# Kernel tuning notes

Measured on AMD Instinct MI355X. Metric: run time of the kernel, lower is better.

Reference implementation:

```python
import jax, jax.numpy as jnp
import numpy as np

C_IN, CH, HCH, NFFT, HOP, NL, K = 100, 512, 1536, 1024, 256, 8, 4
B, T = 16, 1024

def conv1d(x, w, b=None, pad=0, groups=1):
    # x: [B, Cin, L], w: [Cout, Cin/groups, K]
    y = jax.lax.conv_general_dilated(x, w, (1,), [(pad, pad)],
        dimension_numbers=('NCH', 'OIH', 'NCH'), feature_group_count=groups)
    if b is not None:
        y = y + b[None, :, None]
    return y

def layernorm(x, g, b, eps=1e-5):
    # normalize over last axis (channel), torch LayerNorm semantics (biased var)
    mu = jnp.mean(x, -1, keepdims=True)
    var = jnp.var(x, -1, keepdims=True)
    return (x - mu) * jax.lax.rsqrt(var + eps) * g + b

def setup_inputs() -> dict:
    key = jax.random.key(0)
    ks = jax.random.split(key, 8)
    r = lambda k, s: jax.random.normal(k, s, jnp.float32) * 0.02
    return {
        'x': jax.random.normal(ks[0], (B, C_IN, T), jnp.float32),
        'in_w': r(ks[1], (CH, C_IN, 7)), 'in_b': jnp.zeros((CH,), jnp.float32),
        'norm_g': jnp.ones((CH,), jnp.float32), 'norm_b': jnp.zeros((CH,), jnp.float32),
        'dw_w': r(ks[2], (NL, CH, 1, 7)), 'dw_b': jnp.zeros((NL, CH), jnp.float32),
        'ln_g': jnp.ones((NL, CH), jnp.float32), 'ln_b': jnp.zeros((NL, CH), jnp.float32),
        'pw1_w': r(ks[3], (NL, HCH, CH)), 'pw1_b': jnp.zeros((NL, HCH), jnp.float32),
        'pw2_w': r(ks[4], (NL, CH, HCH)), 'pw2_b': jnp.zeros((NL, CH), jnp.float32),
        'ls': jnp.full((NL, CH), 1.0 / NL, jnp.float32),
        'normL_g': jnp.ones((CH,), jnp.float32), 'normL_b': jnp.zeros((CH,), jnp.float32),
        'out_w': r(ks[5], (NFFT, CH, 1)), 'out_b': jnp.zeros((NFFT,), jnp.float32),
        'ov_w': r(ks[6], (HOP, NFFT, K)),
    }

def reference(x, in_w, in_b, norm_g, norm_b, dw_w, dw_b, ln_g, ln_b,
              pw1_w, pw1_b, pw2_w, pw2_b, ls, normL_g, normL_b, out_w, out_b, ov_w):
    x = conv1d(x, in_w, in_b, pad=3)                                   # [B, CH, T]
    x = layernorm(x.transpose(0, 2, 1), norm_g, norm_b).transpose(0, 2, 1)

    def layer(h, p):
        dw, db, g, b, w1, b1, w2, b2, s = p
        y = conv1d(h, dw, db, pad=3, groups=CH)                        # depthwise 7-tap
        y = layernorm(y.transpose(0, 2, 1), g, b)                      # [B, T, CH]
        y = jnp.einsum('btc,hc->bth', y, w1) + b1                      # pointwise expand
        y = jax.nn.gelu(y, approximate=False)
        y = jnp.einsum('bth,ch->btc', y, w2) + b2                      # pointwise project
        return h + (y * s).transpose(0, 2, 1), None

    x, _ = jax.lax.scan(layer, x, (dw_w, dw_b, ln_g, ln_b, pw1_w, pw1_b, pw2_w, pw2_b, ls))
    x = layernorm(x.transpose(0, 2, 1), normL_g, normL_b).transpose(0, 2, 1)
    o = conv1d(x, out_w, out_b, pad=0)                                 # [B, NFFT, T]
    # --- overlap_add ---
    o = conv1d(o, ov_w, None, pad=K - 1)                               # [B, HOP, L], L = T + K - 1
    Bn, C, L = o.shape
    pad_size = C * K - L + K - 1
    o = jnp.pad(o, ((0, 0), (0, 0), (0, pad_size)))
    idx = (jnp.arange(L)[None, :] + jnp.arange(C)[:, None] * (C * K - 1)) % L  # [C, L]
    o = jnp.take_along_axis(o, jnp.broadcast_to(idx[None], (Bn, C, L)), axis=2)
    o = jnp.sum(o, axis=1, keepdims=True)                              # [B, 1, L]
    return o[..., K // 2 : L - K // 2 + 1]                             # [B, 1, T]
```

## Files before the change

### kernel.cpp

```cpp
#include <hip/hip_runtime.h>

#define B_    16
#define CIN   100
#define T_    1024
#define CH_   512
#define HCH_  1536
#define NL_   8
#define NFFT_ 1024
#define HOP_  256
#define BT    (B_ * T_)
#define L_    1027
#define OROWS 1032
#define KIN   704

typedef __bf16 bf16x8 __attribute__((ext_vector_type(8)));
typedef float f32x4 __attribute__((ext_vector_type(4)));
typedef short s16x8 __attribute__((ext_vector_type(8)));
typedef short s16x4 __attribute__((ext_vector_type(4)));

__device__ __forceinline__ short f2b(float f) {
  unsigned u = __float_as_uint(f);
  u += 0x7fffu + ((u >> 16) & 1u);
  return (short)(u >> 16);
}
__device__ __forceinline__ float b2f(short s) {
  return __uint_as_float(((unsigned)(unsigned short)s) << 16);
}

__device__ __forceinline__ float fast_gelu(float x) {
  float ax = fabsf(x);
  float z = 0.7978845608f * ax * (1.f + 0.044715f * ax * ax);
  float e = __expf(-2.f * z);
  float th = 1.f - 2.f * e * __builtin_amdgcn_rcpf(1.f + e);
  float g = copysignf(th, x);
  return 0.5f * x * (1.f + g);
}

__device__ __forceinline__ void gl2lds16(const void* g, void* l) {
  __builtin_amdgcn_global_load_lds(
      (__attribute__((address_space(1))) void*)g,
      (__attribute__((address_space(3))) void*)l, 16, 0, 0);
}

__global__ __launch_bounds__(256) void k_cvt4(const float* __restrict__ s,
                                              short* __restrict__ d, int n4) {
  for (int i = blockIdx.x * 256 + threadIdx.x; i < n4; i += gridDim.x * 256) {
    f32x4 v = *reinterpret_cast<const f32x4*>(&s[i * 4]);
    s16x4 o = {f2b(v[0]), f2b(v[1]), f2b(v[2]), f2b(v[3])};
    *reinterpret_cast<s16x4*>(&d[i * 4]) = o;
  }
}

__global__ __launch_bounds__(256) void k_cvt_ov(const float* __restrict__ w,
                                                short* __restrict__ d) {
  const int n = HOP_ * NFFT_;
  for (int i = blockIdx.x * 256 + threadIdx.x; i < n; i += gridDim.x * 256) {
    f32x4 v = *reinterpret_cast<const f32x4*>(&w[(size_t)i * 4]);
#pragma unroll
    for (int k = 0; k < 4; ++k) d[(size_t)k * n + i] = f2b(v[k]);
  }
}

__global__ __launch_bounds__(256) void k_cvt_inw(const float* __restrict__ w,
                                                 short* __restrict__ d) {
  const int n = CH_ * KIN;
  for (int i = blockIdx.x * 256 + threadIdx.x; i < n; i += gridDim.x * 256) {
    int c = i / KIN, e = i - c * KIN;
    d[i] = (e < 700) ? f2b(w[c * 700 + e]) : (short)0;
  }
}

__global__ __launch_bounds__(256) void k_cvt_dwt(const float* __restrict__ w,
                                                 float* __restrict__ d) {
  const int n = NL_ * 7 * CH_;
  for (int i = blockIdx.x * 256 + threadIdx.x; i < n; i += gridDim.x * 256) {
    int l = i / (7 * CH_), r = i - l * 7 * CH_;
    int k = r >> 9, c = r & 511;
    d[i] = w[((size_t)l * CH_ + c) * 7 + k];
  }
}

__global__ __launch_bounds__(256) void k_im2col(const float* __restrict__ x,
                                                short* __restrict__ xim) {
  const int total = BT * KIN;
  for (int i = blockIdx.x * 256 + threadIdx.x; i < total; i += gridDim.x * 256) {
    int m = i / KIN, e = i - m * KIN;
    int b = m >> 10, t = m & 1023;
    int ci = e / 7, k = e - ci * 7;
    int tt = t + k - 3;
    float v = (e < 700 && tt >= 0 && tt < T_) ? x[((b * CIN + ci) << 10) + tt] : 0.f;
    xim[i] = f2b(v);
  }
}

__global__ __launch_bounds__(256) void k_zeropad(short* __restrict__ o1p) {
  int i = blockIdx.x * 256 + threadIdx.x;
  int b = i >> 13;
  int r8 = (i >> 10) & 7;
  int nn = i & 1023;
  int row = r8 < 4 ? r8 : (OROWS - 8 + r8);
  o1p[((size_t)b * OROWS + row) * NFFT_ + nn] = 0;
}

__global__ __launch_bounds__(256) void k_lnb(const short* __restrict__ in,
                                             short* __restrict__ outp,
                                             const float* __restrict__ g,
                                             const float* __restrict__ bta) {
  int row = blockIdx.x, tid = threadIdx.x;
  unsigned u = *reinterpret_cast<const unsigned*>(&in[(size_t)row * CH_ + tid * 2]);
  float v0 = __uint_as_float(u << 16);
  float v1 = __uint_as_float(u & 0xffff0000u);
  float s = v0 + v1, q = v0 * v0 + v1 * v1;
#pragma unroll
  for (int o = 32; o > 0; o >>= 1) { s += __shfl_down(s, o); q += __shfl_down(q, o); }
  __shared__ float sh[8];
  int wid = tid >> 6, lane = tid & 63;
  if (lane == 0) { sh[wid] = s; sh[wid + 4] = q; }
  __syncthreads();
  float S = sh[0] + sh[1] + sh[2] + sh[3];
  float Q = sh[4] + sh[5] + sh[6] + sh[7];
  float mu  = S * (1.f / 512.f);
  float var = Q * (1.f / 512.f) - mu * mu;
  float r = rsqrtf(var + 1e-5f);
  float x0 = (v0 - mu) * r * g[tid * 2]     + bta[tid * 2];
  float x1 = (v1 - mu) * r * g[tid * 2 + 1] + bta[tid * 2 + 1];
  unsigned o = ((unsigned)(unsigned short)f2b(x0)) |
               (((unsigned)(unsigned short)f2b(x1)) << 16);
  *reinterpret_cast<unsigned*>(&outp[(size_t)row * CH_ + tid * 2]) = o;
}

__global__ __launch_bounds__(256) void k_dwln(const short* __restrict__ h,
                                              const float* __restrict__ dwt,
                                              const float* __restrict__ dwb,
                                              const float* __restrict__ g,
                                              const float* __restrict__ bta,
                                              short* __restrict__ yb) {
  int b = blockIdx.x, t0 = blockIdx.y * 32;
  int tid = threadIdx.x, lane = tid & 63, w = tid >> 6;
  __shared__ short hs[38][512];
  for (int e = tid; e < 38 * 64; e += 256) {
    int row = e >> 6, seg = (e & 63) << 3;
    int t = t0 - 3 + row;
    s16x8 v = {};
    if (t >= 0 && t < T_)
      v = *reinterpret_cast<const s16x8*>(&h[((size_t)((b << 10) + t)) * CH_ + seg]);
    *reinterpret_cast<s16x8*>(&hs[row][seg]) = v;
  }
  const int c0 = lane << 3;
  float wk[7][8];
#pragma unroll
  for (int k = 0; k < 7; ++k) {
    f32x4 lo = *reinterpret_cast<const f32x4*>(&dwt[k * CH_ + c0]);
    f32x4 hi = *reinterpret_cast<const f32x4*>(&dwt[k * CH_ + c0 + 4]);
#pragma unroll
    for (int j = 0; j < 4; ++j) { wk[k][j] = lo[j]; wk[k][j + 4] = hi[j]; }
  }
  float bb[8], gg[8], be[8];
  {
    f32x4 a = *reinterpret_cast<const f32x4*>(&dwb[c0]);
    f32x4 b4 = *reinterpret_cast<const f32x4*>(&dwb[c0 + 4]);
    f32x4 c = *reinterpret_cast<const f32x4*>(&g[c0]);
    f32x4 d = *reinterpret_cast<const f32x4*>(&g[c0 + 4]);
    f32x4 e = *reinterpret_cast<const f32x4*>(&bta[c0]);
    f32x4 f = *reinterpret_cast<const f32x4*>(&bta[c0 + 4]);
#pragma unroll
    for (int j = 0; j < 4; ++j) {
      bb[j] = a[j]; bb[j + 4] = b4[j];
      gg[j] = c[j]; gg[j + 4] = d[j];
      be[j] = e[j]; be[j + 4] = f[j];
    }
  }
  __syncthreads();
#pragma unroll
  for (int i = 0; i < 8; ++i) {
    int r = w * 8 + i;
    float acc[8];
#pragma unroll
    for (int j = 0; j < 8; ++j) acc[j] = bb[j];
#pragma unroll
    for (int k = 0; k < 7; ++k) {
      s16x8 hv = *reinterpret_cast<const s16x8*>(&hs[r + k][c0]);
#pragma unroll
      for (int j = 0; j < 8; ++j) acc[j] += b2f(hv[j]) * wk[k][j];
    }
    float s = 0.f, q = 0.f;
#pragma unroll
    for (int j = 0; j < 8; ++j) { s += acc[j]; q += acc[j] * acc[j]; }
#pragma unroll
    for (int o = 32; o > 0; o >>= 1) { s += __shfl_xor(s, o); q += __shfl_xor(q, o); }
    float mu  = s * (1.f / 512.f);
    float var = q * (1.f / 512.f) - mu * mu;
    float rr = rsqrtf(var + 1e-5f);
    s16x8 ov;
#pragma unroll
    for (int j = 0; j < 8; ++j) ov[j] = f2b((acc[j] - mu) * rr * gg[j] + be[j]);
    *reinterpret_cast<s16x8*>(&yb[((size_t)((b << 10) + t0 + r)) * CH_ + c0]) = ov;
  }
}

template <int MODE>
__global__ __launch_bounds__(256) void k_mgemm(const short* __restrict__ A,
                                               const short* __restrict__ Bw,
                                               const float* __restrict__ bias,
                                               const float* __restrict__ scale,
                                               short* __restrict__ obf,
                                               int N, int K) {
  __shared__ __align__(16) short smem[4 * 128 * 64];
  const int tid = threadIdx.x;
  const int lane = tid & 63, w = tid >> 6;
  const int id = blockIdx.x;
  const int ny = N >> 7;
  const int g8 = id >> 3;
  const int gq = g8 / ny;
  const int mt = (id & 7) + (gq << 3);
  const int nt_ = g8 - gq * ny;
  const int m0 = mt << 7, n0 = nt_ << 7;
  const int wr = (w >> 1) * 64, wc = (w & 1) * 64;
  f32x4 acc[4][4];
#pragma unroll
  for (int i = 0; i < 4; ++i)
#pragma unroll
    for (int j = 0; j < 4; ++j) acc[i][j] = (f32x4){0.f, 0.f, 0.f, 0.f};

  const short* Ab = A + (size_t)m0 * K;
  const short* Bb = Bw + (size_t)n0 * K;
  int r_[4], kk_[4];
#pragma unroll
  for (int j = 0; j < 4; ++j) {
    int c = tid + j * 256;
    r_[j] = c >> 3;
    kk_[j] = (((c & 7) ^ (r_[j] & 7)) * 8);
  }
  const int ar = wr + (lane & 15);
  const int br = wc + (lane & 15);
  const int hi = lane >> 4;
  const int nsteps = K >> 6;

  auto stage = [&](int buf, int k0) {
    short* Sa = smem + buf * 16384;
    short* Sb = Sa + 8192;
#pragma unroll
    for (int j = 0; j < 4; ++j)
      gl2lds16(Ab + (size_t)r_[j] * K + k0 + kk_[j], Sa + (j * 256 + w * 64) * 8);
#pragma unroll
    for (int j = 0; j < 4; ++j)
      gl2lds16(Bb + (size_t)r_[j] * K + k0 + kk_[j], Sb + (j * 256 + w * 64) * 8);
  };

  stage(0, 0);
  asm volatile("s_waitcnt vmcnt(0)" ::: "memory");
  __syncthreads();
  for (int t = 0; t < nsteps; ++t) {
    const int cur = t & 1;
    if (t + 1 < nsteps) stage(cur ^ 1, (t + 1) << 6);
    const short* As = smem + cur * 16384;
    const short* Bs = As + 8192;
#pragma unroll
    for (int ks = 0; ks < 2; ++ks) {
      bf16x8 a[4], b[4];
#pragma unroll
      for (int f = 0; f < 4; ++f) {
        int row = ar + f * 16;
        a[f] = *reinterpret_cast<const bf16x8*>(&As[row * 64 + (((ks * 4 + hi) ^ (row & 7)) * 8)]);
      }
#pragma unroll
      for (int f = 0; f < 4; ++f) {
        int row = br + f * 16;
        b[f] = *reinterpret_cast<const bf16x8*>(&Bs[row * 64 + (((ks * 4 + hi) ^ (row & 7)) * 8)]);
      }
#pragma unroll
      for (int fi = 0; fi < 4; ++fi)
#pragma unroll
        for (int fj = 0; fj < 4; ++fj)
          acc[fi][fj] = __builtin_amdgcn_mfma_f32_16x16x32_bf16(a[fi], b[fj], acc[fi][fj], 0, 0, 0);
    }
    asm volatile("s_waitcnt vmcnt(0)" ::: "memory");
    __syncthreads();
  }
  short* Cl = smem;
  const int colbase = wc + (lane & 15);
#pragma unroll
  for (int fj = 0; fj < 4; ++fj) {
    int cl = colbase + fj * 16;
    int n = n0 + cl;
    float bi = bias[n];
    float sc = (MODE == 2) ? scale[n] : 0.f;
#pragma unroll
    for (int fi = 0; fi < 4; ++fi) {
#pragma unroll
      for (int r = 0; r < 4; ++r) {
        int rl = wr + (hi << 2) + fi * 16 + r;
        float v = acc[fi][fj][r] + bi;
        if (MODE == 1) v = fast_gelu(v);
        if (MODE == 2) v *= sc;
        Cl[rl * 128 + (cl ^ (((rl >> 2) & 3) << 4))] = f2b(v);
      }
    }
  }
  __syncthreads();
  const int cs = (lane & 15) * 8;
#pragma unroll
  for (int it = 0; it < 8; ++it) {
    int rl = w * 32 + it * 4 + (lane >> 4);
    s16x8 v = *reinterpret_cast<const s16x8*>(&Cl[rl * 128 + (cs ^ (((rl >> 2) & 3) << 4))]);
    int m = m0 + rl;
    if (MODE == 2) {
      size_t idx = (size_t)m * N + n0 + cs;
      s16x8 hv = *reinterpret_cast<const s16x8*>(&obf[idx]);
      s16x8 o;
#pragma unroll
      for (int j = 0; j < 8; ++j) o[j] = f2b(b2f(hv[j]) + b2f(v[j]));
      *reinterpret_cast<s16x8*>(&obf[idx]) = o;
    } else if (MODE == 3) {
      int bb = m >> 10, t = m & 1023;
      *reinterpret_cast<s16x8*>(&obf[((size_t)(bb * OROWS + 4 + t)) * NFFT_ + n0 + cs]) = v;
    } else {
      *reinterpret_cast<s16x8*>(&obf[(size_t)m * N + n0 + cs]) = v;
    }
  }
}

__global__ __launch_bounds__(256) void k_ovgemm(const short* __restrict__ o1p,
                                                const short* __restrict__ ovb,
                                                float* __restrict__ o2) {
  __shared__ __align__(16) short As2[2][136 * 64];
  __shared__ __align__(16) short Bs2[2][64 * 64];
  const int tid = threadIdx.x;
  const int lane = tid & 63, w = tid >> 6;
  const int l0 = blockIdx.x * 128, c0 = blockIdx.y * 64, b = blockIdx.z;
  const int wr = (w >> 1) * 64, wc = (w & 1) * 32;
  f32x4 acc[4][2];
#pragma unroll
  for (int i = 0; i < 4; ++i)
#pragma unroll
    for (int j = 0; j < 2; ++j) acc[i][j] = (f32x4){0.f, 0.f, 0.f, 0.f};

  const short* Ab = o1p + (size_t)b * OROWS * NFFT_;
  const int ar = wr + (lane & 15);
  const int br = wc + (lane & 15);
  const int hi = lane >> 4;
  const int sl_row = lane >> 3;
  const int sl_j   = lane & 7;
  int br_[2], bk_[2];
#pragma unroll
  for (int j = 0; j < 2; ++j) {
    int c = tid + j * 256;
    br_[j] = c >> 3;
    bk_[j] = ((c & 7) ^ (br_[j] & 7)) * 8;
  }

  auto stageA = [&](int buf, int k0) {
    for (int cg = w; cg < 17; cg += 4) {
      int lr = cg * 8 + sl_row;
      int gr = l0 + 1 + lr;
      if (gr > OROWS - 1) gr = OROWS - 1;
      int j = sl_j ^ (lr & 7);
      gl2lds16(Ab + (size_t)gr * NFFT_ + k0 + j * 8, &As2[buf][cg * 512]);
    }
  };
  auto stageB = [&](int buf, int k0, int ksh) {
    const short* Bb = ovb + ((size_t)(ksh * HOP_ + c0)) * NFFT_;
#pragma unroll
    for (int j = 0; j < 2; ++j)
      gl2lds16(Bb + (size_t)br_[j] * NFFT_ + k0 + bk_[j],
               &Bs2[buf][(j * 256 + w * 64) * 8]);
  };

  int ab = 0, bb = 0;
  stageA(0, 0);
  stageB(0, 0, 0);
  asm volatile("s_waitcnt vmcnt(0)" ::: "memory");
  __syncthreads();
  for (int t = 0; t < 64; ++t) {
    const int ksh = t & 3;
    const int nt = t + 1;
    if (nt < 64) {
      int nk0 = (nt >> 2) << 6;
      if ((nt & 3) == 0) stageA(ab ^ 1, nk0);
      stageB(bb ^ 1, nk0, nt & 3);
    }
    const short* As = As2[ab];
    const short* Bs = Bs2[bb];
#pragma unroll
    for (int ks = 0; ks < 2; ++ks) {
      bf16x8 a[4], bfr[2];
#pragma unroll
      for (int f = 0; f < 4; ++f) {
        int row = ar + f * 16 + ksh;
        a[f] = *reinterpret_cast<const bf16x8*>(&As[row * 64 + (((ks * 4 + hi) ^ (row & 7)) * 8)]);
      }
#pragma unroll
      for (int f = 0; f < 2; ++f) {
        int row = br + f * 16;
        bfr[f] = *reinterpret_cast<const bf16x8*>(&Bs[row * 64 + (((ks * 4 + hi) ^ (row & 7)) * 8)]);
      }
#pragma unroll
      for (int fi = 0; fi < 4; ++fi)
#pragma unroll
        for (int fj = 0; fj < 2; ++fj)
          acc[fi][fj] = __builtin_amdgcn_mfma_f32_16x16x32_bf16(a[fi], bfr[fj], acc[fi][fj], 0, 0, 0);
    }
    asm volatile("s_waitcnt vmcnt(0)" ::: "memory");
    __syncthreads();
    bb ^= 1;
    if (ksh == 3) ab ^= 1;
  }
  const int lb = l0 + wr + (hi << 2);
  const int cb = c0 + wc + (lane & 15);
#pragma unroll
  for (int fj = 0; fj < 2; ++fj) {
    int c = cb + fj * 16;
#pragma unroll
    for (int fi = 0; fi < 4; ++fi) {
#pragma unroll
      for (int r = 0; r < 4; ++r) {
        int l = lb + fi * 16 + r;
        if (l < L_) o2[((size_t)b * L_ + l) * HOP_ + c] = acc[fi][fj][r];
      }
    }
  }
}

__global__ __launch_bounds__(256) void k_oadd(const float* __restrict__ o2,
                                              float* __restrict__ out) {
  int b = blockIdx.x;
  int t = blockIdx.y * 256 + threadIdx.x;
  int m = t + 2;
  float s = 0.f;
  for (int c = 0; c < HOP_; ++c) {
    s += o2[((size_t)b * L_ + m) * HOP_ + c];
    m -= 4;
    if (m < 0) m += L_;
  }
  out[b * T_ + t] = s;
}

extern "C" void kernel_launch(void* const* d_in, const int* in_sizes, int n_in,
                              void* d_out, int out_size, void* d_ws, size_t ws_size,
                              hipStream_t stream) {
  const float* x      = (const float*)d_in[0];
  const float* in_w   = (const float*)d_in[1];
  const float* in_b   = (const float*)d_in[2];
  const float* norm_g = (const float*)d_in[3];
  const float* norm_b = (const float*)d_in[4];
  const float* dw_w   = (const float*)d_in[5];
  const float* dw_b   = (const float*)d_in[6];
  const float* ln_g   = (const float*)d_in[7];
  const float* ln_b   = (const float*)d_in[8];
  const float* pw1_w  = (const float*)d_in[9];
  const float* pw1_b  = (const float*)d_in[10];
  const float* pw2_w  = (const float*)d_in[11];
  const float* pw2_b  = (const float*)d_in[12];
  const float* ls     = (const float*)d_in[13];
  const float* normLg = (const float*)d_in[14];
  const float* normLb = (const float*)d_in[15];
  const float* out_w  = (const float*)d_in[16];
  const float* out_b  = (const float*)d_in[17];
  const float* ov_w   = (const float*)d_in[18];
  float* out = (float*)d_out;

  char* p = (char*)d_ws;
  short* hb   = (short*)p; p += (size_t)BT * CH_ * 2;
  short* yb   = (short*)p; p += (size_t)BT * CH_ * 2;
  short* zb   = (short*)p; p += (size_t)BT * HCH_ * 2;
  short* pw1b = (short*)p; p += (size_t)NL_ * HCH_ * CH_ * 2;
  short* pw2b = (short*)p; p += (size_t)NL_ * CH_ * HCH_ * 2;
  short* owb  = (short*)p; p += (size_t)NFFT_ * CH_ * 2;
  short* ovb  = (short*)p; p += (size_t)4 * HOP_ * NFFT_ * 2;
  float* dwt  = (float*)p; p += (size_t)NL_ * 7 * CH_ * 4;
  short* xim  = zb;
  short* wib  = zb + (size_t)BT * KIN;
  short* hbL  = yb;
  short* o1p  = zb;
  float* o2   = (float*)hb;

  k_cvt4<<<4096, 256, 0, stream>>>(pw1_w, pw1b, NL_ * HCH_ * CH_ / 4);
  k_cvt4<<<4096, 256, 0, stream>>>(pw2_w, pw2b, NL_ * CH_ * HCH_ / 4);
  k_cvt4<<<512, 256, 0, stream>>>(out_w, owb, NFFT_ * CH_ / 4);
  k_cvt_ov<<<1024, 256, 0, stream>>>(ov_w, ovb);
  k_cvt_inw<<<1408, 256, 0, stream>>>(in_w, wib);
  k_cvt_dwt<<<112, 256, 0, stream>>>(dw_w, dwt);
  k_im2col<<<8192, 256, 0, stream>>>(x, xim);

  k_mgemm<0><<<512, 256, 0, stream>>>(xim, wib, in_b, nullptr, hb, CH_, KIN);
  k_lnb<<<BT, 256, 0, stream>>>(hb, hb, norm_g, norm_b);
  for (int l = 0; l < NL_; ++l) {
    k_dwln<<<dim3(B_, T_ / 32), 256, 0, stream>>>(
        hb, dwt + (size_t)l * 7 * CH_, dw_b + l * CH_,
        ln_g + l * CH_, ln_b + l * CH_, yb);
    k_mgemm<1><<<1536, 256, 0, stream>>>(
        yb, pw1b + (size_t)l * HCH_ * CH_, pw1_b + l * HCH_, nullptr, zb,
        HCH_, CH_);
    k_mgemm<2><<<512, 256, 0, stream>>>(
        zb, pw2b + (size_t)l * CH_ * HCH_, pw2_b + l * CH_, ls + l * CH_, hb,
        CH_, HCH_);
  }
  k_lnb<<<BT, 256, 0, stream>>>(hb, hbL, normLg, normLb);
  k_mgemm<3><<<1024, 256, 0, stream>>>(hbL, owb, out_b, nullptr, o1p, NFFT_, CH_);
  k_zeropad<<<512, 256, 0, stream>>>(o1p);
  k_ovgemm<<<dim3(9, 4, 16), 256, 0, stream>>>(o1p, ovb, o2);
  k_oadd<<<dim3(B_, 4), 256, 0, stream>>>(o2, out);
}
```

Baseline: 885.7 us.

## Add 256x256-tile 512-thread GEMM kernel for pw1 and output projections

Introduces a new GEMM kernel with 256x256 output tiles, 8 waves per block, double-buffered direct global-to-LDS staging and grouped tile ordering. It is used for the pointwise-expand GEMM (with GELU) and the output projection, and the old kernel's GELU and padded-output modes are removed. Larger tiles raise arithmetic intensity and cut the number of A/B reloads. The cost is fewer blocks (384 and 256), which may leave compute units underfilled, and higher register pressure from 32 accumulator fragments per thread.

```diff
diff --git a/kernel.cpp b/kernel.cpp
--- a/kernel.cpp
+++ b/kernel.cpp
@@ -291,7 +291,6 @@
       for (int r = 0; r < 4; ++r) {
         int rl = wr + (hi << 2) + fi * 16 + r;
         float v = acc[fi][fj][r] + bi;
-        if (MODE == 1) v = fast_gelu(v);
         if (MODE == 2) v *= sc;
         Cl[rl * 128 + (cl ^ (((rl >> 2) & 3) << 4))] = f2b(v);
       }
@@ -311,11 +310,133 @@
 #pragma unroll
       for (int j = 0; j < 8; ++j) o[j] = f2b(b2f(hv[j]) + b2f(v[j]));
       *reinterpret_cast<s16x8*>(&obf[idx]) = o;
-    } else if (MODE == 3) {
-      int bb = m >> 10, t = m & 1023;
-      *reinterpret_cast<s16x8*>(&obf[((size_t)(bb * OROWS + 4 + t)) * NFFT_ + n0 + cs]) = v;
     } else {
       *reinterpret_cast<s16x8*>(&obf[(size_t)m * N + n0 + cs]) = v;
+    }
+  }
+}
+
+template <int MODE>
+__global__ __launch_bounds__(512, 2) void k_mg256(const short* __restrict__ A,
+                                                  const short* __restrict__ Bw,
+                                                  const float* __restrict__ bias,
+                                                  short* __restrict__ obf,
+                                                  int N, int K) {
+  constexpr int BM = 256, BN = 256;
+  __shared__ __align__(16) short smem[2 * (BM + BN) * 64];
+  const int tid = threadIdx.x;
+  const int lane = tid & 63, w = tid >> 6;
+  const int wm = w >> 2, wn = w & 3;
+  const int id = blockIdx.x;
+  const int ny = N >> 8;
+  const int g8 = id >> 3, gq = g8 / ny;
+  const int mt = (id & 7) + (gq << 3);
+  const int nt = g8 - gq * ny;
+  const int m0 = mt << 8, n0 = nt << 8;
+
+  f32x4 acc[8][4] = {};
+  const short* Ag = A + (size_t)m0 * K;
+  const short* Bg = Bw + (size_t)n0 * K;
+  short* bufA[2]; short* bufB[2];
+  bufA[0] = smem;                   bufB[0] = smem + BM * 64;
+  bufA[1] = smem + (BM + BN) * 64;  bufB[1] = bufA[1] + BM * 64;
+
+  auto stage = [&](int buf, int k0) {
+#pragma unroll
+    for (int j = 0; j < 4; ++j) {
+      int c = tid + j * 512;
+      int row = c >> 3, ch = (c & 7) ^ (row & 7);
+      gl2lds16(Ag + (size_t)row * K + k0 + ch * 8, bufA[buf] + (j * 512 + w * 64) * 8);
+    }
+#pragma unroll
+    for (int j = 0; j < 4; ++j) {
+      int c = tid + j * 512;
+      int row = c >> 3, ch = (c & 7) ^ (row & 7);
+      gl2lds16(Bg + (size_t)row * K + k0 + ch * 8, bufB[buf] + (j * 512 + w * 64) * 8);
+    }
+  };
+
+  const int nkt = K >> 6;
+  stage(0, 0);
+  stage(1, 64);
+  const int arow0 = wm * 128 + (lane & 15);
+  const int brow0 = wn * 64 + (lane & 15);
+  const int hi = lane >> 4;
+
+  for (int kt = 0; kt < nkt; ++kt) {
+    const int buf = kt & 1;
+    if (kt + 1 < nkt) asm volatile("s_waitcnt vmcnt(8)" ::: "memory");
+    else              asm volatile("s_waitcnt vmcnt(0)" ::: "memory");
+    __builtin_amdgcn_s_barrier();
+    bf16x8 bf[4][2];
+#pragma unroll
+    for (int f = 0; f < 4; ++f)
+#pragma unroll
+      for (int ks = 0; ks < 2; ++ks) {
+        int row = brow0 + f * 16;
+        bf[f][ks] = *reinterpret_cast<const bf16x8*>(
+            &bufB[buf][row * 64 + (((ks * 4 + hi) ^ (row & 7)) * 8)]);
+      }
+#pragma unroll
+    for (int qt = 0; qt < 4; ++qt) {
+      bf16x8 af[2][2];
+#pragma unroll
+      for (int f = 0; f < 2; ++f)
+#pragma unroll
+        for (int ks = 0; ks < 2; ++ks) {
+          int row = arow0 + (qt * 2 + f) * 16;
+          af[f][ks] = *reinterpret_cast<const bf16x8*>(
+              &bufA[buf][row * 64 + (((ks * 4 + hi) ^ (row & 7)) * 8)]);
+        }
+      if (qt == 3) {
+        asm volatile("s_waitcnt lgkmcnt(0)" ::: "memory");
+        __builtin_amdgcn_sched_barrier(0);
+        __builtin_amdgcn_s_barrier();
+        if (kt + 2 < nkt) stage(buf, (kt + 2) << 6);
+      }
+#pragma unroll
+      for (int f = 0; f < 2; ++f)
+#pragma unroll
+        for (int fj = 0; fj < 4; ++fj)
+#pragma unroll
+          for (int ks = 0; ks < 2; ++ks)
+            acc[qt * 2 + f][fj] = __builtin_amdgcn_mfma_f32_16x16x32_bf16(
+                af[f][ks], bf[fj][ks], acc[qt * 2 + f][fj], 0, 0, 0);
+    }
+  }
+  asm volatile("s_waitcnt lgkmcnt(0)" ::: "memory");
+  __builtin_amdgcn_s_barrier();
+  short* Cl = smem;
+  const int clb = wn * 64 + (lane & 15);
+#pragma unroll
+  for (int fj = 0; fj < 4; ++fj) {
+    int cl = clb + fj * 16;
+    float bi = bias[n0 + cl];
+#pragma unroll
+    for (int fi = 0; fi < 8; ++fi) {
+#pragma unroll
+      for (int r = 0; r < 4; ++r) {
+        int rl = wm * 128 + fi * 16 + (hi << 2) + r;
+        float v = acc[fi][fj][r] + bi;
+        if (MODE == 1) v = fast_gelu(v);
+        Cl[rl * 256 + (cl ^ ((rl & 15) << 4))] = f2b(v);
+      }
+    }
+  }
+  __syncthreads();
+#pragma unroll
+  for (int it = 0; it < 16; ++it) {
+    int gc = it * 512 + tid;
+    int row = gc >> 5, ch = gc & 31;
+    int ec = (ch * 8) ^ ((row & 15) << 4);
+    s16x8 v = *reinterpret_cast<const s16x8*>(&Cl[row * 256 + ec]);
+    int m = m0 + row;
+    if (MODE == 3) {
+      int bb = m >> 10, t = m & 1023;
+      *reinterpret_cast<s16x8*>(
+          &obf[((size_t)(bb * OROWS + 4 + t)) * NFFT_ + n0 + ch * 8]) = v;
+    } else {
+      *reinterpret_cast<s16x8*>(&obf[(size_t)m * N + n0 + ch * 8]) = v;
     }
   }
 }
@@ -488,15 +609,14 @@
     k_dwln<<<dim3(B_, T_ / 32), 256, 0, stream>>>(
         hb, dwt + (size_t)l * 7 * CH_, dw_b + l * CH_,
         ln_g + l * CH_, ln_b + l * CH_, yb);
-    k_mgemm<1><<<1536, 256, 0, stream>>>(
-        yb, pw1b + (size_t)l * HCH_ * CH_, pw1_b + l * HCH_, nullptr, zb,
-        HCH_, CH_);
+    k_mg256<1><<<384, 512, 0, stream>>>(
+        yb, pw1b + (size_t)l * HCH_ * CH_, pw1_b + l * HCH_, zb, HCH_, CH_);
     k_mgemm<2><<<512, 256, 0, stream>>>(
         zb, pw2b + (size_t)l * CH_ * HCH_, pw2_b + l * CH_, ls + l * CH_, hb,
         CH_, HCH_);
   }
   k_lnb<<<BT, 256, 0, stream>>>(hb, hbL, normLg, normLb);
-  k_mgemm<3><<<1024, 256, 0, stream>>>(hbL, owb, out_b, nullptr, o1p, NFFT_, CH_);
+  k_mg256<3><<<256, 512, 0, stream>>>(hbL, owb, out_b, o1p, NFFT_, CH_);
   k_zeropad<<<512, 256, 0, stream>>>(o1p);
   k_ovgemm<<<dim3(9, 4, 16), 256, 0, stream>>>(o1p, ovb, o2);
   k_oadd<<<dim3(B_, 4), 256, 0, stream>>>(o2, out);
```

Measured after the change: 1.050 ms. 18.5% more time.
